# Optimization experiments

Measured on AMD Instinct MI355X. Metric: run time of the kernel, lower is better.

## Reference

```python
import jax, jax.numpy as jnp
import numpy as np

H = 512  # hidden_size

def _cell_step(carry, x, W_ih, b_ih, W_hh):
    h, c = carry
    v = x @ W_ih.T + b_ih + h @ W_hh.T            # [B, 4H]
    i, f, g, o = jnp.split(v, 4, axis=1)
    new_c = jax.nn.sigmoid(f) * c + jax.nn.sigmoid(i) * jnp.tanh(g)
    new_h = jnp.tanh(new_c) * jax.nn.sigmoid(o)
    return (new_h, new_c), new_h

def setup_inputs() -> dict:
    key = jax.random.key(0)
    ks = jax.random.split(key, 8)
    B, T, D = 32, 512, 512
    inputs_emb = jax.random.normal(ks[0], (B, T, D), dtype=jnp.float32)
    mask = jax.random.randint(ks[1], (B, T), 0, 2).astype(jnp.int32)
    s = 1.0 / np.sqrt(D)
    W_ih_f = jax.random.normal(ks[2], (4 * H, D), dtype=jnp.float32) * s
    b_ih_f = jnp.zeros((4 * H,), dtype=jnp.float32)
    W_hh_f = jax.random.normal(ks[3], (4 * H, H), dtype=jnp.float32) * s
    W_ih_b = jax.random.normal(ks[4], (4 * H, D), dtype=jnp.float32) * s
    b_ih_b = jnp.zeros((4 * H,), dtype=jnp.float32)
    W_hh_b = jax.random.normal(ks[5], (4 * H, H), dtype=jnp.float32) * s
    return {"inputs_emb": inputs_emb, "mask": mask,
            "W_ih_f": W_ih_f, "b_ih_f": b_ih_f, "W_hh_f": W_hh_f,
            "W_ih_b": W_ih_b, "b_ih_b": b_ih_b, "W_hh_b": W_hh_b}

def reference(inputs_emb, mask, W_ih_f, b_ih_f, W_hh_f, W_ih_b, b_ih_b, W_hh_b):
    B, T, D = inputs_emb.shape
    h0 = jnp.zeros((B, H), dtype=inputs_emb.dtype)
    c0 = jnp.zeros((B, H), dtype=inputs_emb.dtype)

    xs = jnp.transpose(inputs_emb, (1, 0, 2))  # [T, B, D]
    step_f = lambda carry, x: _cell_step(carry, x, W_ih_f, b_ih_f, W_hh_f)
    _, out_f = jax.lax.scan(step_f, (h0, c0), xs)          # [T, B, H]
    out_f = jnp.transpose(out_f, (1, 0, 2))                # [B, T, H]

    # Rotation indices: sentence of length L -> index_b = (arange(T)+L) % T,
    # index_f = (arange(T)+(T-L)) % T  (matches torch list construction).
    lengths = jnp.sum(mask.astype(jnp.int32), axis=1)      # [B]
    ar = jnp.arange(T)[None, :]                            # [1, T]
    index_b = (ar + lengths[:, None]) % T                  # [B, T]
    index_f = (ar + (T - lengths)[:, None]) % T            # [B, T]

    inputs_rot = jnp.take_along_axis(inputs_emb, index_b[:, :, None], axis=1)
    xs_b = jnp.transpose(inputs_rot, (1, 0, 2))            # [T, B, D]
    step_b = lambda carry, x: _cell_step(carry, x, W_ih_b, b_ih_b, W_hh_b)
    _, out_b = jax.lax.scan(step_b, (h0, c0), xs_b, reverse=True)  # [T, B, H]
    out_b = jnp.transpose(out_b, (1, 0, 2))                # [B, T, H]
    out_b = jnp.take_along_axis(out_b, index_f[:, :, None], axis=1)

    return jnp.concatenate([out_f, out_b], axis=-1)        # [B, T, 2H]
```

## Files before the change

kernel.cpp:

```cpp
#include <hip/hip_runtime.h>
#include <hip/hip_bf16.h>


typedef __bf16 bf16;
typedef __attribute__((ext_vector_type(8))) __bf16 bf16x8;
typedef __attribute__((ext_vector_type(4))) float f32x4;
typedef unsigned long long u64;

__device__ __forceinline__ float sigmoidf_(float x) {
  return 1.f / (1.f + __expf(-x));
}
__device__ __forceinline__ float tanhf_(float x) {
  float e = __expf(-2.f * fabsf(x));
  return copysignf((1.f - e) / (1.f + e), x);
}
__device__ __forceinline__ u64 ald64(const u64* p) {
  return __hip_atomic_load(p, __ATOMIC_RELAXED, __HIP_MEMORY_SCOPE_AGENT);
}
__device__ __forceinline__ void ast64(u64* p, u64 v) {
  __hip_atomic_store(p, v, __ATOMIC_RELAXED, __HIP_MEMORY_SCOPE_AGENT);
}
__device__ __forceinline__ bf16x8 cvt8v(float4 a, float4 b) {
  bf16x8 v;
  v[0] = (bf16)a.x; v[1] = (bf16)a.y; v[2] = (bf16)a.z; v[3] = (bf16)a.w;
  v[4] = (bf16)b.x; v[5] = (bf16)b.y; v[6] = (bf16)b.z; v[7] = (bf16)b.w;
  return v;
}
__device__ __forceinline__ void bar_lgkm() {
  asm volatile("s_waitcnt lgkmcnt(0)\n\ts_barrier" ::: "memory");
}

__global__ void lengths_kernel(const int* __restrict__ mask, int* __restrict__ lengths) {
  __shared__ int part[32][8];
  int t = threadIdx.x;
  int b = t >> 3, sub = t & 7;
  int s = 0;
#pragma unroll 8
  for (int k = 0; k < 64; ++k) s += mask[b * 512 + sub + 8 * k];
  part[b][sub] = s;
  __syncthreads();
  if (sub == 0) {
    int tot = 0;
#pragma unroll
    for (int k = 0; k < 8; ++k) tot += part[b][k];
    lengths[b] = tot;
  }
}

__global__ __launch_bounds__(256, 1) void lstm_fused(
    const float* __restrict__ x,
    const float* __restrict__ Wih_f, const float* __restrict__ bih_f,
    const float* __restrict__ Whh_f,
    const float* __restrict__ Wih_b, const float* __restrict__ bih_b,
    const float* __restrict__ Whh_b,
    const int* __restrict__ lengths,
    u64* __restrict__ hbuf,
    float* __restrict__ out) {
  const int s = blockIdx.x;
  const int dir = blockIdx.y;
  const int grp = blockIdx.z;
  const float* Wih = dir ? Wih_b : Wih_f;
  const float* Whh = dir ? Whh_b : Whh_f;
  const float* bih = dir ? bih_b : bih_f;
  const int b0 = grp * 16;

  const int tid = threadIdx.x;
  const int lane = tid & 63, wave = tid >> 6;
  const int l15 = lane & 15, quad = lane >> 4;

  __shared__ __align__(16) bf16 xA[2][16 * 512];
  __shared__ __align__(16) bf16 hA[16 * 512];
  __shared__ float vbuf[4][16][17];
  __shared__ int lenL[16];

  bf16x8 wih[16], whh[16];
  {
    int grow = wave * 512 + s * 16 + l15;
#pragma unroll
    for (int k = 0; k < 16; ++k) {
      const float* pw = Wih + (size_t)grow * 512 + k * 32 + quad * 8;
      const float* ph = Whh + (size_t)grow * 512 + k * 32 + quad * 8;
      wih[k] = cvt8v(*(const float4*)pw, *(const float4*)(pw + 4));
      whh[k] = cvt8v(*(const float4*)ph, *(const float4*)(ph + 4));
    }
  }
  const float bv = bih[wave * 512 + s * 16 + l15];
  if (tid < 16) lenL[tid] = lengths[b0 + tid];
  __syncthreads();

  const int cb = tid >> 3, cj = (tid & 7) * 2;
  int lenR[4];
#pragma unroll
  for (int i = 0; i < 4; ++i) lenR[i] = lenL[(i * 256 + tid) >> 6];
  const int lenO = (tid < 128) ? lenL[cb] : 0;

  float creg0 = 0.f, creg1 = 0.f;
  u64* hb = hbuf + (size_t)dir * (2 * 32 * 256);

  float4 xp[4][2];
#pragma unroll
  for (int i = 0; i < 4; ++i) {
    int c = i * 256 + tid;
    int m = c >> 6, kbp = c & 63;
    int kb = kbp ^ (m & 7);
    int tr = (dir == 0) ? 0 : ((511 + lenR[i]) & 511);
    const float4* p = (const float4*)(x + ((size_t)(b0 + m) * 512 + tr) * 512 + kb * 8);
    xp[i][0] = p[0]; xp[i][1] = p[1];
  }
#pragma unroll
  for (int i = 0; i < 4; ++i) {
    int c = i * 256 + tid;
    *(bf16x8*)(xA[0] + c * 8) = cvt8v(xp[i][0], xp[i][1]);
  }
#pragma unroll
  for (int i = 0; i < 4; ++i) {
    int c = i * 256 + tid;
    int m = c >> 6, kbp = c & 63;
    int kb = kbp ^ (m & 7);
    int tr = (dir == 0) ? 1 : ((510 + lenR[i]) & 511);
    const float4* p = (const float4*)(x + ((size_t)(b0 + m) * 512 + tr) * 512 + kb * 8);
    xp[i][0] = p[0]; xp[i][1] = p[1];
  }
  bar_lgkm();

  for (int step = 0; step < 512; ++step) {
    const int par = step & 1;
    const u64* hprev = hb + (size_t)par * (32 * 256);
    u64* hnext = hb + (size_t)(par ^ 1) * (32 * 256);
    const bf16* xcur = xA[par];
    bf16* xnxt = xA[par ^ 1];

    if (step < 511) {
#pragma unroll
      for (int i = 0; i < 4; ++i) {
        int c = i * 256 + tid;
        *(bf16x8*)(xnxt + c * 8) = cvt8v(xp[i][0], xp[i][1]);
      }
    }
    if (step < 510) {
#pragma unroll
      for (int i = 0; i < 4; ++i) {
        int c = i * 256 + tid;
        int m = c >> 6, kbp = c & 63;
        int kb = kbp ^ (m & 7);
        int tr = (dir == 0) ? (step + 2) : ((509 - step + lenR[i]) & 511);
        const float4* p = (const float4*)(x + ((size_t)(b0 + m) * 512 + tr) * 512 + kb * 8);
        xp[i][0] = p[0]; xp[i][1] = p[1];
      }
    }

    f32x4 acc0 = {bv, bv, bv, bv};
#pragma unroll
    for (int k = 0; k < 16; ++k) {
      int kb = k * 4 + quad;
      int sw = (kb ^ (l15 & 7)) * 8;
      bf16x8 ax0 = *(const bf16x8*)(xcur + l15 * 512 + sw);
      acc0 = __builtin_amdgcn_mfma_f32_16x16x32_bf16(ax0, wih[k], acc0, 0, 0, 0);
    }
    __builtin_amdgcn_sched_barrier(0);

    u64 hv[4][4];
    {
      const unsigned target = (unsigned)step;
      while (true) {
#pragma unroll
        for (int b = 0; b < 4; ++b) {
          const u64* rp = hprev + (size_t)(b0 + wave * 4 + b) * 256 + lane;
#pragma unroll
          for (int j = 0; j < 4; ++j) hv[b][j] = ald64(rp + 64 * j);
        }
        int ok = 1;
#pragma unroll
        for (int b = 0; b < 4; ++b)
#pragma unroll
          for (int j = 0; j < 4; ++j)
            ok &= (int)((unsigned)(hv[b][j] >> 32) >= target);
        if (__all(ok)) break;
        __builtin_amdgcn_s_sleep(1);
      }
    }

#pragma unroll
    for (int b = 0; b < 4; ++b) {
      int m = wave * 4 + b;
#pragma unroll
      for (int j = 0; j < 4; ++j) {
        int b8 = (lane >> 2) + 16 * j;
        int b8s = b8 ^ (m & 7);
        *(unsigned*)(hA + m * 512 + b8s * 8 + 2 * (lane & 3)) = (unsigned)hv[b][j];
      }
    }
    bar_lgkm();

#pragma unroll
    for (int k = 0; k < 16; ++k) {
      int kb = k * 4 + quad;
      int sw = (kb ^ (l15 & 7)) * 8;
      bf16x8 ah0 = *(const bf16x8*)(hA + l15 * 512 + sw);
      acc0 = __builtin_amdgcn_mfma_f32_16x16x32_bf16(ah0, whh[k], acc0, 0, 0, 0);
    }
#pragma unroll
    for (int r = 0; r < 4; ++r)
      vbuf[wave][quad * 4 + r][l15] = acc0[r];
    bar_lgkm();

    if (tid < 128) {
      float i0 = vbuf[0][cb][cj],     f0 = vbuf[1][cb][cj];
      float g0 = vbuf[2][cb][cj],     o0 = vbuf[3][cb][cj];
      float i1 = vbuf[0][cb][cj + 1], f1 = vbuf[1][cb][cj + 1];
      float g1 = vbuf[2][cb][cj + 1], o1 = vbuf[3][cb][cj + 1];
      float c0 = sigmoidf_(f0) * creg0 + sigmoidf_(i0) * tanhf_(g0);
      float c1 = sigmoidf_(f1) * creg1 + sigmoidf_(i1) * tanhf_(g1);
      creg0 = c0; creg1 = c1;
      float h0 = tanhf_(c0) * sigmoidf_(o0);
      float h1 = tanhf_(c1) * sigmoidf_(o1);

      unsigned ulo = (unsigned)__builtin_bit_cast(unsigned short, (bf16)h0);
      unsigned uhi = (unsigned)__builtin_bit_cast(unsigned short, (bf16)h1);
      u64 pk = ((u64)(unsigned)(step + 1) << 32) | (u64)(ulo | (uhi << 16));
      ast64(hnext + (size_t)(b0 + cb) * 256 + s * 8 + (tid & 7), pk);

      int tr = (dir == 0) ? step : ((511 - step + lenO) & 511);
      *(float2*)(out + (size_t)((b0 + cb) * 512 + tr) * 1024 + dir * 512 + s * 16 + cj) =
          make_float2(h0, h1);
    }
  }
}

extern "C" void kernel_launch(void* const* d_in, const int* in_sizes, int n_in,
                              void* d_out, int out_size, void* d_ws, size_t ws_size,
                              hipStream_t stream) {
  (void)in_sizes; (void)n_in; (void)out_size; (void)ws_size;
  const float* x    = (const float*)d_in[0];
  const int*   mask = (const int*)  d_in[1];
  const float* Wihf = (const float*)d_in[2];
  const float* bihf = (const float*)d_in[3];
  const float* Whhf = (const float*)d_in[4];
  const float* Wihb = (const float*)d_in[5];
  const float* bihb = (const float*)d_in[6];
  const float* Whhb = (const float*)d_in[7];
  float* out = (float*)d_out;

  char* ws = (char*)d_ws;
  u64* hbuf = (u64*)ws;
  int* lengths = (int*)(ws + 262144);
  const size_t head = 262144;

  hipMemsetAsync(d_ws, 0, head, stream);
  lengths_kernel<<<1, 256, 0, stream>>>(mask, lengths);
  lstm_fused<<<dim3(32, 2, 2), 256, 0, stream>>>(
      x, Wihf, bihf, Whhf, Wihb, bihb, Whhb, lengths, hbuf, out);
}
```

Before: 1.850 ms.

## Split batch into groups of four per block to quadruple grid parallelism

Each block now handles 4 batch rows instead of 16, and the grid's batch-group dimension grows from 2 to 8, giving 512 blocks with launch bounds allowing 2 per CU. The unused MFMA rows in the shared x and h tiles are zeroed once, and the per-step x prefetch, h spin-wait and cell update shrink to one row per wave. The aim is to spread the serial recurrence across more CUs and cut per-block work on the critical path. In exchange every block still loads the full weight slice into registers and runs the same count of MFMAs with three quarters of the rows wasted. There are also 4x more blocks spinning on the global h-buffer flags, and all 512 must be co-resident or the kernel deadlocks.

New measurement: 1.917 ms. 3.6% more time.

```diff
diff --git a/kernel.cpp b/kernel.cpp
--- a/kernel.cpp
+++ b/kernel.cpp
@@ -47,7 +47,7 @@
   }
 }
 
-__global__ __launch_bounds__(256, 1) void lstm_fused(
+__global__ __launch_bounds__(256, 2) void lstm_fused(
     const float* __restrict__ x,
     const float* __restrict__ Wih_f, const float* __restrict__ bih_f,
     const float* __restrict__ Whh_f,
@@ -62,7 +62,7 @@
   const float* Wih = dir ? Wih_b : Wih_f;
   const float* Whh = dir ? Whh_b : Whh_f;
   const float* bih = dir ? bih_b : bih_f;
-  const int b0 = grp * 16;
+  const int b0 = grp * 4;
 
   const int tid = threadIdx.x;
   const int lane = tid & 63, wave = tid >> 6;
@@ -71,7 +71,7 @@
   __shared__ __align__(16) bf16 xA[2][16 * 512];
   __shared__ __align__(16) bf16 hA[16 * 512];
   __shared__ float vbuf[4][16][17];
-  __shared__ int lenL[16];
+  __shared__ int lenL[4];
 
   bf16x8 wih[16], whh[16];
   {
@@ -85,41 +85,38 @@
     }
   }
   const float bv = bih[wave * 512 + s * 16 + l15];
-  if (tid < 16) lenL[tid] = lengths[b0 + tid];
+  if (tid < 4) lenL[tid] = lengths[b0 + tid];
+
+  {
+    for (int c = tid; c < 2304; c += 256) {
+      int buf = c / 768, rc = c - buf * 768;
+      int r = rc >> 6, off = (rc & 63) * 8;
+      bf16* dst = (buf == 0) ? (xA[0] + (4 + r) * 512 + off)
+                : (buf == 1) ? (xA[1] + (4 + r) * 512 + off)
+                             : (hA + (4 + r) * 512 + off);
+      *(ulonglong2*)dst = make_ulonglong2(0ull, 0ull);
+    }
+  }
   __syncthreads();
 
   const int cb = tid >> 3, cj = (tid & 7) * 2;
-  int lenR[4];
-#pragma unroll
-  for (int i = 0; i < 4; ++i) lenR[i] = lenL[(i * 256 + tid) >> 6];
-  const int lenO = (tid < 128) ? lenL[cb] : 0;
+  const int lenR0 = lenL[tid >> 6];
+  const int lenO = (tid < 32) ? lenL[cb] : 0;
 
   float creg0 = 0.f, creg1 = 0.f;
   u64* hb = hbuf + (size_t)dir * (2 * 32 * 256);
 
-  float4 xp[4][2];
-#pragma unroll
-  for (int i = 0; i < 4; ++i) {
-    int c = i * 256 + tid;
-    int m = c >> 6, kbp = c & 63;
+  float4 xp0, xp1;
+  {
+    int m = tid >> 6, kbp = tid & 63;
     int kb = kbp ^ (m & 7);
-    int tr = (dir == 0) ? 0 : ((511 + lenR[i]) & 511);
+    int tr = (dir == 0) ? 0 : ((511 + lenR0) & 511);
     const float4* p = (const float4*)(x + ((size_t)(b0 + m) * 512 + tr) * 512 + kb * 8);
-    xp[i][0] = p[0]; xp[i][1] = p[1];
-  }
-#pragma unroll
-  for (int i = 0; i < 4; ++i) {
-    int c = i * 256 + tid;
-    *(bf16x8*)(xA[0] + c * 8) = cvt8v(xp[i][0], xp[i][1]);
-  }
-#pragma unroll
-  for (int i = 0; i < 4; ++i) {
-    int c = i * 256 + tid;
-    int m = c >> 6, kbp = c & 63;
-    int kb = kbp ^ (m & 7);
-    int tr = (dir == 0) ? 1 : ((510 + lenR[i]) & 511);
-    const float4* p = (const float4*)(x + ((size_t)(b0 + m) * 512 + tr) * 512 + kb * 8);
-    xp[i][0] = p[0]; xp[i][1] = p[1];
+    xp0 = p[0]; xp1 = p[1];
+    *(bf16x8*)(xA[0] + tid * 8) = cvt8v(xp0, xp1);
+    tr = (dir == 0) ? 1 : ((510 + lenR0) & 511);
+    p = (const float4*)(x + ((size_t)(b0 + m) * 512 + tr) * 512 + kb * 8);
+    xp0 = p[0]; xp1 = p[1];
   }
   bar_lgkm();
 
@@ -131,22 +128,14 @@
     bf16* xnxt = xA[par ^ 1];
 
     if (step < 511) {
-#pragma unroll
-      for (int i = 0; i < 4; ++i) {
-        int c = i * 256 + tid;
-        *(bf16x8*)(xnxt + c * 8) = cvt8v(xp[i][0], xp[i][1]);
-      }
+      *(bf16x8*)(xnxt + tid * 8) = cvt8v(xp0, xp1);
     }
     if (step < 510) {
-#pragma unroll
-      for (int i = 0; i < 4; ++i) {
-        int c = i * 256 + tid;
-        int m = c >> 6, kbp = c & 63;
-        int kb = kbp ^ (m & 7);
-        int tr = (dir == 0) ? (step + 2) : ((509 - step + lenR[i]) & 511);
-        const float4* p = (const float4*)(x + ((size_t)(b0 + m) * 512 + tr) * 512 + kb * 8);
-        xp[i][0] = p[0]; xp[i][1] = p[1];
-      }
+      int m = tid >> 6, kbp = tid & 63;
+      int kb = kbp ^ (m & 7);
+      int tr = (dir == 0) ? (step + 2) : ((509 - step + lenR0) & 511);
+      const float4* p = (const float4*)(x + ((size_t)(b0 + m) * 512 + tr) * 512 + kb * 8);
+      xp0 = p[0]; xp1 = p[1];
     }
 
     f32x4 acc0 = {bv, bv, bv, bv};
@@ -159,35 +148,29 @@
     }
     __builtin_amdgcn_sched_barrier(0);
 
-    u64 hv[4][4];
+    u64 hv[4];
     {
       const unsigned target = (unsigned)step;
+      const u64* rp = hprev + (size_t)(b0 + wave) * 256 + lane;
       while (true) {
 #pragma unroll
-        for (int b = 0; b < 4; ++b) {
-          const u64* rp = hprev + (size_t)(b0 + wave * 4 + b) * 256 + lane;
-#pragma unroll
-          for (int j = 0; j < 4; ++j) hv[b][j] = ald64(rp + 64 * j);
-        }
+        for (int j = 0; j < 4; ++j) hv[j] = ald64(rp + 64 * j);
         int ok = 1;
 #pragma unroll
-        for (int b = 0; b < 4; ++b)
-#pragma unroll
-          for (int j = 0; j < 4; ++j)
-            ok &= (int)((unsigned)(hv[b][j] >> 32) >= target);
+        for (int j = 0; j < 4; ++j)
+          ok &= (int)((unsigned)(hv[j] >> 32) >= target);
         if (__all(ok)) break;
         __builtin_amdgcn_s_sleep(1);
       }
     }
 
-#pragma unroll
-    for (int b = 0; b < 4; ++b) {
-      int m = wave * 4 + b;
+    {
+      int m = wave;
 #pragma unroll
       for (int j = 0; j < 4; ++j) {
         int b8 = (lane >> 2) + 16 * j;
         int b8s = b8 ^ (m & 7);
-        *(unsigned*)(hA + m * 512 + b8s * 8 + 2 * (lane & 3)) = (unsigned)hv[b][j];
+        *(unsigned*)(hA + m * 512 + b8s * 8 + 2 * (lane & 3)) = (unsigned)hv[j];
       }
     }
     bar_lgkm();
@@ -204,7 +187,7 @@
       vbuf[wave][quad * 4 + r][l15] = acc0[r];
     bar_lgkm();
 
-    if (tid < 128) {
+    if (tid < 32) {
       float i0 = vbuf[0][cb][cj],     f0 = vbuf[1][cb][cj];
       float g0 = vbuf[2][cb][cj],     o0 = vbuf[3][cb][cj];
       float i1 = vbuf[0][cb][cj + 1], f1 = vbuf[1][cb][cj + 1];
@@ -248,6 +231,6 @@
 
   hipMemsetAsync(d_ws, 0, head, stream);
   lengths_kernel<<<1, 256, 0, stream>>>(mask, lengths);
-  lstm_fused<<<dim3(32, 2, 2), 256, 0, stream>>>(
+  lstm_fused<<<dim3(32, 2, 8), 256, 0, stream>>>(
       x, Wihf, bihf, Whhf, Wihb, bihb, Whhb, lengths, hbuf, out);
 }
```
